# Kernel optimization log

Hardware: AMD Instinct MI355X
Metric: run time of the kernel (lower is better)

The kernel has to match this reference:

```python
import jax, jax.numpy as jnp
import numpy as np

EPS = 1e-12  # config.layer_norm_eps (BERT default)

N, E, H, L = 64, 64, 768, 512


def setup_inputs() -> dict:
    key = jax.random.key(0)
    k1, k2 = jax.random.split(key)
    nodes_state = jax.random.normal(k1, (N, E, H), dtype=jnp.float32)
    # mapping weights (e.g., soft node->token assignment), non-negative
    nodes_mapping = jax.random.uniform(k2, (N, E, L), dtype=jnp.float32)
    gamma = jnp.ones((H,), dtype=jnp.float32)
    beta = jnp.zeros((H,), dtype=jnp.float32)
    return {"nodes_state": nodes_state, "nodes_mapping": nodes_mapping,
            "gamma": gamma, "beta": beta}


def _layer_norm(x, gamma, beta):
    mu = jnp.mean(x, axis=-1, keepdims=True)
    var = jnp.mean(jnp.square(x - mu), axis=-1, keepdims=True)
    return (x - mu) * jax.lax.rsqrt(var + EPS) * gamma + beta


def reference(nodes_state, nodes_mapping, gamma, beta):
    # sum_e nodes_state[n,e,:,h] * nodes_mapping[n,e,l,:]  ==  mapping^T @ state
    # (N,E,H) x (N,E,L) -> (N,L,H), batched matmul instead of N*E*L*H intermediate
    expand = jnp.einsum('neh,nel->nlh', nodes_state, nodes_mapping)
    return _layer_norm(expand, gamma, beta)
```

## Files before the change

kernel.cpp:

```cpp
#include <hip/hip_runtime.h>
#include <hip/hip_bf16.h>

#define Nn 64
#define Ee 64
#define Hh 768
#define Ll 512
#define NEH (Nn * Ee * Hh)
#define NEL (Nn * Ee * Ll)

typedef __attribute__((ext_vector_type(8))) short bf16x8;
typedef __attribute__((ext_vector_type(4))) float f32x4;

__global__ __launch_bounds__(256) void cvt_transpose(
    const float* __restrict__ state, const float* __restrict__ mapping,
    __hip_bfloat16* __restrict__ sT, __hip_bfloat16* __restrict__ mT)
{
    __shared__ unsigned short lds[64][66];

    int b = blockIdx.x;
    const float* src;
    __hip_bfloat16* dst;
    int W, x0;
    if (b < Nn * (Hh / 64)) {
        int n = b / (Hh / 64);
        x0 = (b % (Hh / 64)) * 64;
        src = state + (size_t)n * Ee * Hh;
        dst = sT + (size_t)n * Hh * Ee;
        W = Hh;
    } else {
        b -= Nn * (Hh / 64);
        int n = b / (Ll / 64);
        x0 = (b % (Ll / 64)) * 64;
        src = mapping + (size_t)n * Ee * Ll;
        dst = mT + (size_t)n * Ll * Ee;
        W = Ll;
    }

    const int xr = (threadIdx.x & 31) * 2;
    const int er = threadIdx.x >> 5;
#pragma unroll
    for (int i = 0; i < 8; ++i) {
        int e = i * 8 + er;
        float2 v = *reinterpret_cast<const float2*>(src + (size_t)e * W + x0 + xr);
        union { __hip_bfloat16 b16; unsigned short u; } c0, c1;
        c0.b16 = __float2bfloat16(v.x);
        c1.b16 = __float2bfloat16(v.y);
        lds[xr][e]     = c0.u;
        lds[xr + 1][e] = c1.u;
    }
    __syncthreads();

    const int e4 = (threadIdx.x & 15) * 4;
    const int xw = threadIdx.x >> 4;
    unsigned short* dsts = reinterpret_cast<unsigned short*>(dst);
#pragma unroll
    for (int i = 0; i < 4; ++i) {
        int x = i * 16 + xw;
        uint2 v;
        v.x = *reinterpret_cast<const unsigned int*>(&lds[x][e4]);
        v.y = *reinterpret_cast<const unsigned int*>(&lds[x][e4 + 2]);
        *reinterpret_cast<uint2*>(dsts + (size_t)(x0 + x) * Ee + e4) = v;
    }
}

__global__ __launch_bounds__(256) void gemm_ln(
    const __hip_bfloat16* __restrict__ sT,
    const __hip_bfloat16* __restrict__ mT,
    const float* __restrict__ gamma,
    const float* __restrict__ beta,
    float* __restrict__ out)
{
    const int p    = blockIdx.x;
    const int n    = ((p >> 7) << 3) | (p & 7);
    const int l0   = ((p >> 3) & 15) << 5;
    const int tid  = threadIdx.x;
    const int w    = tid >> 6;
    const int lane = tid & 63;
    const int g    = lane >> 4;
    const int c    = lane & 15;

    bf16x8 b0[2], b1[2];
#pragma unroll
    for (int u = 0; u < 2; ++u) {
        const __hip_bfloat16* Brow = mT + (size_t)(n * Ll + l0 + u * 16 + c) * Ee + g * 8;
        b0[u] = *reinterpret_cast<const bf16x8*>(Brow);
        b1[u] = *reinterpret_cast<const bf16x8*>(Brow + 32);
    }

    f32x4 acc[12][2];
#pragma unroll
    for (int t = 0; t < 12; ++t)
#pragma unroll
        for (int u = 0; u < 2; ++u) acc[t][u] = (f32x4){0.f, 0.f, 0.f, 0.f};

    const __hip_bfloat16* Abase = sT + (size_t)(n * Hh + w * 192 + c) * Ee + g * 8;
#pragma unroll
    for (int t = 0; t < 12; ++t) {
        const __hip_bfloat16* ap = Abase + (size_t)t * 16 * Ee;
        bf16x8 a0 = *reinterpret_cast<const bf16x8*>(ap);
        bf16x8 a1 = *reinterpret_cast<const bf16x8*>(ap + 32);
#pragma unroll
        for (int u = 0; u < 2; ++u) {
            acc[t][u] = __builtin_amdgcn_mfma_f32_16x16x32_bf16(a0, b0[u], acc[t][u], 0, 0, 0);
            acc[t][u] = __builtin_amdgcn_mfma_f32_16x16x32_bf16(a1, b1[u], acc[t][u], 0, 0, 0);
        }
    }

    float s[2] = {0.f, 0.f}, q[2] = {0.f, 0.f};
#pragma unroll
    for (int t = 0; t < 12; ++t)
#pragma unroll
        for (int u = 0; u < 2; ++u)
#pragma unroll
            for (int r = 0; r < 4; ++r) {
                float v = acc[t][u][r];
                s[u] += v;
                q[u] += v * v;
            }
#pragma unroll
    for (int off = 16; off < 64; off <<= 1)
#pragma unroll
        for (int u = 0; u < 2; ++u) {
            s[u] += __shfl_xor(s[u], off, 64);
            q[u] += __shfl_xor(q[u], off, 64);
        }
    __shared__ float redS[32][4];
    __shared__ float redQ[32][4];
    if (g == 0) {
#pragma unroll
        for (int u = 0; u < 2; ++u) {
            redS[u * 16 + c][w] = s[u];
            redQ[u * 16 + c][w] = q[u];
        }
    }
    __syncthreads();

    float mu[2], rstd[2];
#pragma unroll
    for (int u = 0; u < 2; ++u) {
        int li = u * 16 + c;
        float S = redS[li][0] + redS[li][1] + redS[li][2] + redS[li][3];
        float Q = redQ[li][0] + redQ[li][1] + redQ[li][2] + redQ[li][3];
        float m = S * (1.f / Hh);
        float v = Q * (1.f / Hh) - m * m;
        mu[u]   = m;
        rstd[u] = rsqrtf(v + 1e-12f);
    }

#pragma unroll
    for (int t = 0; t < 12; ++t) {
        int hb = w * 192 + t * 16 + g * 4;
        f32x4 gm = *reinterpret_cast<const f32x4*>(gamma + hb);
        f32x4 bt = *reinterpret_cast<const f32x4*>(beta + hb);
#pragma unroll
        for (int u = 0; u < 2; ++u) {
            f32x4 v;
#pragma unroll
            for (int r = 0; r < 4; ++r)
                v[r] = (acc[t][u][r] - mu[u]) * rstd[u] * gm[r] + bt[r];
            *reinterpret_cast<f32x4*>(
                out + (size_t)(n * Ll + l0 + u * 16 + c) * Hh + hb) = v;
        }
    }
}

extern "C" void kernel_launch(void* const* d_in, const int* in_sizes, int n_in,
                              void* d_out, int out_size, void* d_ws, size_t ws_size,
                              hipStream_t stream)
{
    const float* state   = (const float*)d_in[0];
    const float* mapping = (const float*)d_in[1];
    const float* gamma   = (const float*)d_in[2];
    const float* beta    = (const float*)d_in[3];
    float* out           = (float*)d_out;

    __hip_bfloat16* sT = (__hip_bfloat16*)d_ws;
    __hip_bfloat16* mT = sT + NEH;

    const int tiles = Nn * (Hh / 64) + Nn * (Ll / 64);
    cvt_transpose<<<tiles, 256, 0, stream>>>(state, mapping, sT, mT);
    gemm_ln<<<Nn * (Ll / 32), 256, 0, stream>>>(sT, mT, gamma, beta, out);
}
```

Baseline: 43.10 us.

## Fuse bf16 conversion and transpose into the GEMM+LayerNorm kernel via LDS staging

Removes the separate convert/transpose kernel and workspace. Each block now loads fp32 state and mapping directly, converts them to bf16 into transposed LDS tiles, and runs the MFMA GEMM in two K-halves before the LayerNorm. This avoids a kernel launch and the bf16 workspace write/read. In exchange, every block re-reads the full fp32 state slice for its batch, raising cache traffic, and the large LDS allocation limits occupancy.

Result: slower. 48.61 us (+12.8%).

```diff
diff --git a/kernel.cpp b/kernel.cpp
--- a/kernel.cpp
+++ b/kernel.cpp
@@ -5,71 +5,31 @@
 #define Ee 64
 #define Hh 768
 #define Ll 512
-#define NEH (Nn * Ee * Hh)
-#define NEL (Nn * Ee * Ll)
 
 typedef __attribute__((ext_vector_type(8))) short bf16x8;
 typedef __attribute__((ext_vector_type(4))) float f32x4;
 
-__global__ __launch_bounds__(256) void cvt_transpose(
-    const float* __restrict__ state, const float* __restrict__ mapping,
-    __hip_bfloat16* __restrict__ sT, __hip_bfloat16* __restrict__ mT)
-{
-    __shared__ unsigned short lds[64][66];
+#define SROW 40
+#define MROW 72
 
-    int b = blockIdx.x;
-    const float* src;
-    __hip_bfloat16* dst;
-    int W, x0;
-    if (b < Nn * (Hh / 64)) {
-        int n = b / (Hh / 64);
-        x0 = (b % (Hh / 64)) * 64;
-        src = state + (size_t)n * Ee * Hh;
-        dst = sT + (size_t)n * Hh * Ee;
-        W = Hh;
-    } else {
-        b -= Nn * (Hh / 64);
-        int n = b / (Ll / 64);
-        x0 = (b % (Ll / 64)) * 64;
-        src = mapping + (size_t)n * Ee * Ll;
-        dst = mT + (size_t)n * Ll * Ee;
-        W = Ll;
-    }
-
-    const int xr = (threadIdx.x & 31) * 2;
-    const int er = threadIdx.x >> 5;
-#pragma unroll
-    for (int i = 0; i < 8; ++i) {
-        int e = i * 8 + er;
-        float2 v = *reinterpret_cast<const float2*>(src + (size_t)e * W + x0 + xr);
-        union { __hip_bfloat16 b16; unsigned short u; } c0, c1;
-        c0.b16 = __float2bfloat16(v.x);
-        c1.b16 = __float2bfloat16(v.y);
-        lds[xr][e]     = c0.u;
-        lds[xr + 1][e] = c1.u;
-    }
-    __syncthreads();
-
-    const int e4 = (threadIdx.x & 15) * 4;
-    const int xw = threadIdx.x >> 4;
-    unsigned short* dsts = reinterpret_cast<unsigned short*>(dst);
-#pragma unroll
-    for (int i = 0; i < 4; ++i) {
-        int x = i * 16 + xw;
-        uint2 v;
-        v.x = *reinterpret_cast<const unsigned int*>(&lds[x][e4]);
-        v.y = *reinterpret_cast<const unsigned int*>(&lds[x][e4 + 2]);
-        *reinterpret_cast<uint2*>(dsts + (size_t)(x0 + x) * Ee + e4) = v;
-    }
+__device__ __forceinline__ unsigned short f2bf(float x) {
+    union { __hip_bfloat16 b; unsigned short u; } cv;
+    cv.b = __float2bfloat16(x);
+    return cv.u;
 }
 
-__global__ __launch_bounds__(256) void gemm_ln(
-    const __hip_bfloat16* __restrict__ sT,
-    const __hip_bfloat16* __restrict__ mT,
+__global__ __launch_bounds__(256, 2) void fused_expand_ln(
+    const float* __restrict__ state,
+    const float* __restrict__ mapping,
     const float* __restrict__ gamma,
     const float* __restrict__ beta,
     float* __restrict__ out)
 {
+    __shared__ unsigned short sS[4][192][SROW];
+    __shared__ unsigned short sM[32][MROW];
+    __shared__ float redS[32][4];
+    __shared__ float redQ[32][4];
+
     const int p    = blockIdx.x;
     const int n    = ((p >> 7) << 3) | (p & 7);
     const int l0   = ((p >> 3) & 15) << 5;
@@ -79,13 +39,35 @@
     const int g    = lane >> 4;
     const int c    = lane & 15;
 
-    bf16x8 b0[2], b1[2];
+    const float* stn = state   + (size_t)n * (Ee * Hh);
+    const float* mpn = mapping + (size_t)n * (Ee * Ll);
+
 #pragma unroll
-    for (int u = 0; u < 2; ++u) {
-        const __hip_bfloat16* Brow = mT + (size_t)(n * Ll + l0 + u * 16 + c) * Ee + g * 8;
-        b0[u] = *reinterpret_cast<const bf16x8*>(Brow);
-        b1[u] = *reinterpret_cast<const bf16x8*>(Brow + 32);
+    for (int i = 0; i < 2; ++i) {
+        int idx = i * 256 + tid;
+        int e   = idx >> 3;
+        int lq  = idx & 7;
+        float4 v = *reinterpret_cast<const float4*>(mpn + (size_t)e * Ll + l0 + lq * 4);
+        sM[lq * 4 + 0][e] = f2bf(v.x);
+        sM[lq * 4 + 1][e] = f2bf(v.y);
+        sM[lq * 4 + 2][e] = f2bf(v.z);
+        sM[lq * 4 + 3][e] = f2bf(v.w);
     }
+
+    const int se = lane & 31;
+    const int hh = (lane >> 5) * 96;
+    {
+        const float* sp = stn + (size_t)se * Hh + w * 192 + hh;
+#pragma unroll
+        for (int x = 0; x < 24; ++x) {
+            float4 v = *reinterpret_cast<const float4*>(sp + x * 4);
+            sS[w][hh + x * 4 + 0][se] = f2bf(v.x);
+            sS[w][hh + x * 4 + 1][se] = f2bf(v.y);
+            sS[w][hh + x * 4 + 2][se] = f2bf(v.z);
+            sS[w][hh + x * 4 + 3][se] = f2bf(v.w);
+        }
+    }
+    __syncthreads();
 
     f32x4 acc[12][2];
 #pragma unroll
@@ -93,16 +75,45 @@
 #pragma unroll
         for (int u = 0; u < 2; ++u) acc[t][u] = (f32x4){0.f, 0.f, 0.f, 0.f};
 
-    const __hip_bfloat16* Abase = sT + (size_t)(n * Hh + w * 192 + c) * Ee + g * 8;
+    {
+        bf16x8 b[2];
 #pragma unroll
-    for (int t = 0; t < 12; ++t) {
-        const __hip_bfloat16* ap = Abase + (size_t)t * 16 * Ee;
-        bf16x8 a0 = *reinterpret_cast<const bf16x8*>(ap);
-        bf16x8 a1 = *reinterpret_cast<const bf16x8*>(ap + 32);
+        for (int u = 0; u < 2; ++u)
+            b[u] = *reinterpret_cast<const bf16x8*>(&sM[u * 16 + c][g * 8]);
 #pragma unroll
-        for (int u = 0; u < 2; ++u) {
-            acc[t][u] = __builtin_amdgcn_mfma_f32_16x16x32_bf16(a0, b0[u], acc[t][u], 0, 0, 0);
-            acc[t][u] = __builtin_amdgcn_mfma_f32_16x16x32_bf16(a1, b1[u], acc[t][u], 0, 0, 0);
+        for (int t = 0; t < 12; ++t) {
+            bf16x8 a = *reinterpret_cast<const bf16x8*>(&sS[w][t * 16 + c][g * 8]);
+#pragma unroll
+            for (int u = 0; u < 2; ++u)
+                acc[t][u] = __builtin_amdgcn_mfma_f32_16x16x32_bf16(a, b[u], acc[t][u], 0, 0, 0);
+        }
+    }
+    __syncthreads();
+
+    {
+        const float* sp = stn + (size_t)(32 + se) * Hh + w * 192 + hh;
+#pragma unroll
+        for (int x = 0; x < 24; ++x) {
+            float4 v = *reinterpret_cast<const float4*>(sp + x * 4);
+            sS[w][hh + x * 4 + 0][se] = f2bf(v.x);
+            sS[w][hh + x * 4 + 1][se] = f2bf(v.y);
+            sS[w][hh + x * 4 + 2][se] = f2bf(v.z);
+            sS[w][hh + x * 4 + 3][se] = f2bf(v.w);
+        }
+    }
+    __syncthreads();
+
+    {
+        bf16x8 b[2];
+#pragma unroll
+        for (int u = 0; u < 2; ++u)
+            b[u] = *reinterpret_cast<const bf16x8*>(&sM[u * 16 + c][32 + g * 8]);
+#pragma unroll
+        for (int t = 0; t < 12; ++t) {
+            bf16x8 a = *reinterpret_cast<const bf16x8*>(&sS[w][t * 16 + c][g * 8]);
+#pragma unroll
+            for (int u = 0; u < 2; ++u)
+                acc[t][u] = __builtin_amdgcn_mfma_f32_16x16x32_bf16(a, b[u], acc[t][u], 0, 0, 0);
         }
     }
 
@@ -124,8 +135,6 @@
             s[u] += __shfl_xor(s[u], off, 64);
             q[u] += __shfl_xor(q[u], off, 64);
         }
-    __shared__ float redS[32][4];
-    __shared__ float redQ[32][4];
     if (g == 0) {
 #pragma unroll
         for (int u = 0; u < 2; ++u) {
@@ -174,10 +183,5 @@
     const float* beta    = (const float*)d_in[3];
     float* out           = (float*)d_out;
 
-    __hip_bfloat16* sT = (__hip_bfloat16*)d_ws;
-    __hip_bfloat16* mT = sT + NEH;
-
-    const int tiles = Nn * (Hh / 64) + Nn * (Ll / 64);
-    cvt_transpose<<<tiles, 256, 0, stream>>>(state, mapping, sT, mT);
-    gemm_ln<<<Nn * (Ll / 32), 256, 0, stream>>>(sT, mT, gamma, beta, out);
+    fused_expand_ln<<<Nn * (Ll / 32), 256, 0, stream>>>(state, mapping, gamma, beta, out);
 }
```

## Split GEMM+LayerNorm into stats pass and recompute-and-store pass

Applied to the files above, without the earlier changes.

Splits the fused GEMM+LayerNorm kernel in two. A first kernel computes per-row mean and rstd into a workspace buffer. A second kernel recomputes each 16-column MFMA tile on the fly, normalizes it and stores it. This removes the large per-thread accumulator array, cutting register pressure so stores can stream per tile. The cost is doing the GEMM and its operand loads twice, plus an extra kernel launch.

Result: slower. 52.44 us (+21.7%).

```diff
diff --git a/kernel.cpp b/kernel.cpp
--- a/kernel.cpp
+++ b/kernel.cpp
@@ -63,13 +63,14 @@
     }
 }
 
-__global__ __launch_bounds__(256) void gemm_ln(
+__global__ __launch_bounds__(256) void stats_pass(
     const __hip_bfloat16* __restrict__ sT,
     const __hip_bfloat16* __restrict__ mT,
-    const float* __restrict__ gamma,
-    const float* __restrict__ beta,
-    float* __restrict__ out)
-{
+    float2* __restrict__ stats)
+{
+    __shared__ float redS[32][4];
+    __shared__ float redQ[32][4];
+
     const int p    = blockIdx.x;
     const int n    = ((p >> 7) << 3) | (p & 7);
     const int l0   = ((p >> 3) & 15) << 5;
@@ -124,8 +125,6 @@
             s[u] += __shfl_xor(s[u], off, 64);
             q[u] += __shfl_xor(q[u], off, 64);
         }
-    __shared__ float redS[32][4];
-    __shared__ float redQ[32][4];
     if (g == 0) {
 #pragma unroll
         for (int u = 0; u < 2; ++u) {
@@ -135,31 +134,70 @@
     }
     __syncthreads();
 
-    float mu[2], rstd[2];
+    if (tid < 16) {
+#pragma unroll
+        for (int u = 0; u < 2; ++u) {
+            int li = u * 16 + c;
+            float S = redS[li][0] + redS[li][1] + redS[li][2] + redS[li][3];
+            float Q = redQ[li][0] + redQ[li][1] + redQ[li][2] + redQ[li][3];
+            float m = S * (1.f / Hh);
+            float v = Q * (1.f / Hh) - m * m;
+            stats[n * Ll + l0 + li] = make_float2(m, rsqrtf(v + 1e-12f));
+        }
+    }
+}
+
+__global__ __launch_bounds__(256) void gemm_store(
+    const __hip_bfloat16* __restrict__ sT,
+    const __hip_bfloat16* __restrict__ mT,
+    const float2* __restrict__ stats,
+    const float* __restrict__ gamma,
+    const float* __restrict__ beta,
+    float* __restrict__ out)
+{
+    const int p    = blockIdx.x;
+    const int n    = ((p >> 7) << 3) | (p & 7);
+    const int l0   = ((p >> 3) & 15) << 5;
+    const int tid  = threadIdx.x;
+    const int w    = tid >> 6;
+    const int lane = tid & 63;
+    const int g    = lane >> 4;
+    const int c    = lane & 15;
+
+    bf16x8 b0[2], b1[2];
+    float2 st[2];
+    float* orow[2];
 #pragma unroll
     for (int u = 0; u < 2; ++u) {
-        int li = u * 16 + c;
-        float S = redS[li][0] + redS[li][1] + redS[li][2] + redS[li][3];
-        float Q = redQ[li][0] + redQ[li][1] + redQ[li][2] + redQ[li][3];
-        float m = S * (1.f / Hh);
-        float v = Q * (1.f / Hh) - m * m;
-        mu[u]   = m;
-        rstd[u] = rsqrtf(v + 1e-12f);
-    }
-
-#pragma unroll
+        const int l = l0 + u * 16 + c;
+        const __hip_bfloat16* Brow = mT + (size_t)(n * Ll + l) * Ee + g * 8;
+        b0[u] = *reinterpret_cast<const bf16x8*>(Brow);
+        b1[u] = *reinterpret_cast<const bf16x8*>(Brow + 32);
+        st[u] = stats[n * Ll + l];
+        orow[u] = out + (size_t)(n * Ll + l) * Hh;
+    }
+
+    const __hip_bfloat16* Abase = sT + (size_t)(n * Hh + w * 192 + c) * Ee + g * 8;
+#pragma unroll 1
     for (int t = 0; t < 12; ++t) {
-        int hb = w * 192 + t * 16 + g * 4;
+        const __hip_bfloat16* ap = Abase + (size_t)t * 16 * Ee;
+        bf16x8 a0 = *reinterpret_cast<const bf16x8*>(ap);
+        bf16x8 a1 = *reinterpret_cast<const bf16x8*>(ap + 32);
+
+        const int hb = w * 192 + t * 16 + g * 4;
         f32x4 gm = *reinterpret_cast<const f32x4*>(gamma + hb);
         f32x4 bt = *reinterpret_cast<const f32x4*>(beta + hb);
-#pragma unroll
-        for (int u = 0; u < 2; ++u) {
+
+#pragma unroll
+        for (int u = 0; u < 2; ++u) {
+            f32x4 acc = (f32x4){0.f, 0.f, 0.f, 0.f};
+            acc = __builtin_amdgcn_mfma_f32_16x16x32_bf16(a0, b0[u], acc, 0, 0, 0);
+            acc = __builtin_amdgcn_mfma_f32_16x16x32_bf16(a1, b1[u], acc, 0, 0, 0);
             f32x4 v;
 #pragma unroll
             for (int r = 0; r < 4; ++r)
-                v[r] = (acc[t][u][r] - mu[u]) * rstd[u] * gm[r] + bt[r];
-            *reinterpret_cast<f32x4*>(
-                out + (size_t)(n * Ll + l0 + u * 16 + c) * Hh + hb) = v;
+                v[r] = (acc[r] - st[u].x) * st[u].y * gm[r] + bt[r];
+            *reinterpret_cast<f32x4*>(orow[u] + hb) = v;
         }
     }
 }
@@ -176,8 +214,10 @@
 
     __hip_bfloat16* sT = (__hip_bfloat16*)d_ws;
     __hip_bfloat16* mT = sT + NEH;
+    float2* stats      = (float2*)(mT + NEL);
 
     const int tiles = Nn * (Hh / 64) + Nn * (Ll / 64);
     cvt_transpose<<<tiles, 256, 0, stream>>>(state, mapping, sT, mT);
-    gemm_ln<<<Nn * (Ll / 32), 256, 0, stream>>>(sT, mT, gamma, beta, out);
-}
+    stats_pass<<<Nn * (Ll / 32), 256, 0, stream>>>(sT, mT, stats);
+    gemm_store<<<Nn * (Ll / 32), 256, 0, stream>>>(sT, mT, stats, gamma, beta, out);
+}
```
